# Kernel tuning notes

Measured on AMD Instinct MI355X. Metric: run time of the kernel, lower is better.

## Reference

```python
import jax, jax.numpy as jnp
import numpy as np

D_MODEL = 256
OUT_DIM = 256
D_STATE = 16
D_CONV = 4
EXPAND = 2
D_INNER = EXPAND * D_MODEL  # 512
DT_RANK = (D_MODEL + 15) // 16  # 16
B_SZ, L = 2, 4096


def setup_inputs() -> dict:
    key = jax.random.key(0)
    ks = jax.random.split(key, 12)
    s = lambda *sh: 0.02
    inp = {}
    inp['x'] = jax.random.normal(ks[0], (B_SZ, L, D_MODEL), jnp.float32)
    inp['ln_w'] = jnp.ones((D_MODEL,), jnp.float32)
    inp['ln_b'] = jnp.zeros((D_MODEL,), jnp.float32)
    inp['in_proj_w'] = jax.random.normal(ks[1], (2 * D_INNER, D_MODEL), jnp.float32) * 0.02
    inp['conv_w'] = jax.random.normal(ks[2], (D_INNER, 1, D_CONV), jnp.float32) * 0.2
    inp['conv_b'] = jnp.zeros((D_INNER,), jnp.float32)
    inp['x_proj_w'] = jax.random.normal(ks[3], (DT_RANK + 2 * D_STATE, D_INNER), jnp.float32) * 0.02
    inp['dt_proj_w'] = jax.random.normal(ks[4], (D_INNER, DT_RANK), jnp.float32) * 0.05
    inp['dt_proj_b'] = jax.random.uniform(ks[5], (D_INNER,), jnp.float32, -4.0, -2.0)  # small dt after softplus
    inp['A_log'] = jnp.log(jnp.broadcast_to(jnp.arange(1, D_STATE + 1, dtype=jnp.float32), (D_INNER, D_STATE)))
    inp['Dskip'] = jnp.ones((D_INNER,), jnp.float32)
    inp['out_proj_w'] = jax.random.normal(ks[6], (D_MODEL, D_INNER), jnp.float32) * 0.02
    inp['proj_w'] = jax.random.normal(ks[7], (OUT_DIM, D_MODEL), jnp.float32) * 0.02
    inp['proj_b'] = jnp.zeros((OUT_DIM,), jnp.float32)
    inp['skip_scale'] = jnp.ones((1,), jnp.float32)
    return inp


def _layernorm(x, w, b, eps=1e-5):
    mu = jnp.mean(x, axis=-1, keepdims=True)
    var = jnp.var(x, axis=-1, keepdims=True)
    return (x - mu) * jax.lax.rsqrt(var + eps) * w + b


def _selective_scan(u, delta, A, Bm, Cm, Dskip):
    # u, delta: (B,L,d); A: (d,n); Bm, Cm: (B,L,n)
    dA = jnp.exp(delta[..., None] * A)                       # (B,L,d,n)
    dBu = (delta * u)[..., None] * Bm[:, :, None, :]          # (B,L,d,n)
    h0 = jnp.zeros((u.shape[0], A.shape[0], A.shape[1]), u.dtype)

    def step(h, inp):
        dA_t, dBu_t, C_t = inp
        h = dA_t * h + dBu_t                                  # (B,d,n)
        y = jnp.einsum('bdn,bn->bd', h, C_t)
        return h, y

    xs = (dA.transpose(1, 0, 2, 3), dBu.transpose(1, 0, 2, 3), Cm.transpose(1, 0, 2))
    _, ys = jax.lax.scan(step, h0, xs)                        # (L,B,d)
    return ys.transpose(1, 0, 2) + u * Dskip


def _mamba(xn, in_proj_w, conv_w, conv_b, x_proj_w, dt_proj_w, dt_proj_b, A_log, Dskip, out_proj_w):
    # xn: (B,L,d_model)
    xz = jnp.einsum('bld,ed->ble', xn, in_proj_w)             # (B,L,2*d_inner)
    xi, z = jnp.split(xz, 2, axis=-1)
    # depthwise causal conv over L
    xc = jax.lax.conv_general_dilated(
        xi.transpose(0, 2, 1), conv_w, window_strides=(1,),
        padding=[(D_CONV - 1, 0)], feature_group_count=D_INNER,
        dimension_numbers=('NCH', 'OIH', 'NCH'))
    xc = (xc + conv_b[None, :, None]).transpose(0, 2, 1)       # (B,L,d_inner)
    xc = jax.nn.silu(xc)
    dbc = jnp.einsum('bld,ed->ble', xc, x_proj_w)             # (B,L,dt_rank+2n)
    dt, Bm, Cm = jnp.split(dbc, [DT_RANK, DT_RANK + D_STATE], axis=-1)
    delta = jax.nn.softplus(jnp.einsum('blr,dr->bld', dt, dt_proj_w) + dt_proj_b)
    A = -jnp.exp(A_log)                                       # (d_inner, n)
    y = _selective_scan(xc, delta, A, Bm, Cm, Dskip)
    y = y * jax.nn.silu(z)
    return jnp.einsum('ble,de->bld', y, out_proj_w)


def reference(x, ln_w, ln_b, in_proj_w, conv_w, conv_b, x_proj_w, dt_proj_w, dt_proj_b,
              A_log, Dskip, out_proj_w, proj_w, proj_b, skip_scale):
    x_norm = _layernorm(x, ln_w, ln_b)
    x_mamba = _mamba(x_norm, in_proj_w, conv_w, conv_b, x_proj_w, dt_proj_w, dt_proj_b,
                     A_log, Dskip, out_proj_w) + skip_scale * x
    x_mamba = _layernorm(x_mamba, ln_w, ln_b)
    return jnp.einsum('bld,od->blo', x_mamba, proj_w) + proj_b
```

## Files before the change

kernel.cpp:

```cpp
#include <hip/hip_runtime.h>
#include <hip/hip_bf16.h>

#define B_SZ   2
#define LSEQ   4096
#define NCH    256
#define CL     16
#define DROWS  16

typedef __attribute__((ext_vector_type(8))) short short8;
typedef __attribute__((ext_vector_type(4))) float f32x4;

__device__ __forceinline__ unsigned short f2bf(float f) {
  union { float f; unsigned u; } x; x.f = f;
  unsigned r = x.u + 0x7fffu + ((x.u >> 16) & 1u);
  return (unsigned short)(r >> 16);
}
__device__ __forceinline__ float bf2f(unsigned short u) {
  union { unsigned u; float f; } x; x.u = (unsigned)u << 16;
  return x.f;
}

__device__ __forceinline__ void gload_lds16(const unsigned short* g, unsigned short* l) {
  __builtin_amdgcn_global_load_lds(
      (const __attribute__((address_space(1))) unsigned int*)g,
      (__attribute__((address_space(3))) unsigned int*)l, 16, 0, 0);
}

__global__ __launch_bounds__(256) void prep_kernel(
    const float* __restrict__ x, const float* __restrict__ ln_w,
    const float* __restrict__ ln_b, unsigned short* __restrict__ xn_bf,
    const float* __restrict__ inW,  unsigned short* __restrict__ inW_bf,
    const float* __restrict__ outW, unsigned short* __restrict__ outW_bf,
    const float* __restrict__ projW, unsigned short* __restrict__ projW_bf,
    const float* __restrict__ xprojW, unsigned short* __restrict__ xprojW_bf,
    const float* __restrict__ A_log, float* __restrict__ Ar_tab)
{
  if (blockIdx.x < 2048) {
    int wv = threadIdx.x >> 6, lane = threadIdx.x & 63;
    size_t row = (size_t)blockIdx.x * 4 + wv;
    float4 v = reinterpret_cast<const float4*>(x)[row * 64 + lane];
    float s  = v.x + v.y + v.z + v.w;
    float sq = v.x*v.x + v.y*v.y + v.z*v.z + v.w*v.w;
    #pragma unroll
    for (int off = 32; off; off >>= 1) {
      s  += __shfl_xor(s,  off);
      sq += __shfl_xor(sq, off);
    }
    float mu  = s * (1.f/256.f);
    float var = sq * (1.f/256.f) - mu*mu;
    float rs  = rsqrtf(var + 1e-5f);
    float4 wv4 = reinterpret_cast<const float4*>(ln_w)[lane];
    float4 bv4 = reinterpret_cast<const float4*>(ln_b)[lane];
    ushort4 o;
    o.x = f2bf((v.x-mu)*rs*wv4.x + bv4.x);
    o.y = f2bf((v.y-mu)*rs*wv4.y + bv4.y);
    o.z = f2bf((v.z-mu)*rs*wv4.z + bv4.z);
    o.w = f2bf((v.w-mu)*rs*wv4.w + bv4.w);
    reinterpret_cast<ushort4*>(xn_bf)[row * 64 + lane] = o;
    return;
  }
  int j = (blockIdx.x - 2048) * 256 + threadIdx.x;
  const float* src; unsigned short* dst; int off;
  if (j < 65536)       { src = inW;    dst = inW_bf;    off = j; }
  else if (j < 98304)  { src = outW;   dst = outW_bf;   off = j - 65536; }
  else if (j < 114688) { src = projW;  dst = projW_bf;  off = j - 98304; }
  else if (j < 120832) { src = xprojW; dst = xprojW_bf; off = j - 114688; }
  else {
    int a = (j - 120832) * 4;
    float4 v = *reinterpret_cast<const float4*>(A_log + a);
    float4 o = {-__expf(v.x), -__expf(v.y), -__expf(v.z), -__expf(v.w)};
    *reinterpret_cast<float4*>(Ar_tab + a) = o;
    return;
  }
  float4 v = *reinterpret_cast<const float4*>(src + off*4);
  ushort4 o;
  o.x = f2bf(v.x); o.y = f2bf(v.y); o.z = f2bf(v.z); o.w = f2bf(v.w);
  *reinterpret_cast<ushort4*>(dst + off*4) = o;
}

__global__ __launch_bounds__(256) void ln_bf16_kernel(
    const unsigned short* __restrict__ in, const float* __restrict__ w,
    const float* __restrict__ b, unsigned short* __restrict__ out)
{
  int wv = threadIdx.x >> 6, lane = threadIdx.x & 63;
  size_t row = (size_t)blockIdx.x * 4 + wv;
  ushort4 uv = reinterpret_cast<const ushort4*>(in)[row * 64 + lane];
  float4 v = {bf2f(uv.x), bf2f(uv.y), bf2f(uv.z), bf2f(uv.w)};
  float s  = v.x + v.y + v.z + v.w;
  float sq = v.x*v.x + v.y*v.y + v.z*v.z + v.w*v.w;
  #pragma unroll
  for (int off = 32; off; off >>= 1) {
    s  += __shfl_xor(s,  off);
    sq += __shfl_xor(sq, off);
  }
  float mu  = s * (1.f/256.f);
  float var = sq * (1.f/256.f) - mu*mu;
  float rs  = rsqrtf(var + 1e-5f);
  float4 wv4 = reinterpret_cast<const float4*>(w)[lane];
  float4 bv4 = reinterpret_cast<const float4*>(b)[lane];
  ushort4 o;
  o.x = f2bf((v.x-mu)*rs*wv4.x + bv4.x);
  o.y = f2bf((v.y-mu)*rs*wv4.y + bv4.y);
  o.z = f2bf((v.z-mu)*rs*wv4.z + bv4.z);
  o.w = f2bf((v.w-mu)*rs*wv4.w + bv4.w);
  reinterpret_cast<ushort4*>(out)[row * 64 + lane] = o;
}

enum { EPI_NONE = 0, EPI_SKIPX = 1, EPI_BIAS = 2 };

template<int BM, int BN, int EPI, typename OT>
__global__ __launch_bounds__(256) void gemm_mfma(
    const unsigned short* __restrict__ A, const unsigned short* __restrict__ W,
    OT* __restrict__ C, int M, int N, int K,
    const float* __restrict__ X, const float* __restrict__ sscale,
    const float* __restrict__ bias)
{
  constexpr int BK = 32;
  constexpr int WM = BM / 2, WN = BN / 2;
  constexpr int AM = WM / 16, BF = WN / 16;
  constexpr int AI = BM / 64, BI = BN / 64;
  __shared__ __align__(16) unsigned short As[2][BM * BK];
  __shared__ __align__(16) unsigned short Ws[2][BN * BK];
  const int tid = threadIdx.x, lane = tid & 63, wid = tid >> 6;
  const int wr = wid >> 1, wc = wid & 1;
  const int bm = blockIdx.x * BM, bn = blockIdx.y * BN;
  const int srow = lane >> 2;
  const int skoff = (lane & 3) * 8;

  f32x4 acc[AM][BF] = {};

  auto stage = [&](int buf, int kt) {
    #pragma unroll
    for (int i = 0; i < AI; i++) {
      int rowg = (wid * AI + i) * 16;
      gload_lds16(A + (size_t)(bm + rowg + srow) * K + kt + skoff,
                  &As[buf][rowg * BK]);
    }
    #pragma unroll
    for (int i = 0; i < BI; i++) {
      int rowg = (wid * BI + i) * 16;
      gload_lds16(W + (size_t)(bn + rowg + srow) * K + kt + skoff,
                  &Ws[buf][rowg * BK]);
    }
  };

  stage(0, 0);
  __syncthreads();
  const int nt = K / BK;
  int cur = 0;
  for (int t = 0; t < nt; t++) {
    if (t + 1 < nt) stage(cur ^ 1, (t + 1) * BK);
    short8 af[AM], bfr[BF];
    #pragma unroll
    for (int i = 0; i < AM; i++)
      af[i] = *reinterpret_cast<const short8*>(
          &As[cur][(wr * WM + i * 16 + (lane & 15)) * BK + (lane >> 4) * 8]);
    #pragma unroll
    for (int j = 0; j < BF; j++)
      bfr[j] = *reinterpret_cast<const short8*>(
          &Ws[cur][(wc * WN + j * 16 + (lane & 15)) * BK + (lane >> 4) * 8]);
    #pragma unroll
    for (int i = 0; i < AM; i++)
      #pragma unroll
      for (int j = 0; j < BF; j++)
        acc[i][j] = __builtin_amdgcn_mfma_f32_16x16x32_bf16(af[i], bfr[j], acc[i][j], 0, 0, 0);
    __syncthreads();
    cur ^= 1;
  }

  float sv = 0.f;
  if constexpr (EPI == EPI_SKIPX) sv = sscale[0];

  #pragma unroll
  for (int i = 0; i < AM; i++) {
    #pragma unroll
    for (int j = 0; j < BF; j++) {
      int row0 = bm + wr * WM + i * 16 + ((lane >> 4) << 2);
      int col  = bn + wc * WN + j * 16 + (lane & 15);
      #pragma unroll
      for (int r = 0; r < 4; r++) {
        float v = acc[i][j][r];
        size_t off = (size_t)(row0 + r) * N + col;
        if constexpr (EPI == EPI_SKIPX) v += sv * X[off];
        if constexpr (EPI == EPI_BIAS)  v += bias[col];
        if constexpr (sizeof(OT) == 2) C[off] = (OT)f2bf(v);
        else                           C[off] = v;
      }
    }
  }
}

__global__ __launch_bounds__(256) void gemm_mfma48(
    const unsigned short* __restrict__ A, const unsigned short* __restrict__ W,
    float* __restrict__ C, int K)
{
  __shared__ __align__(16) unsigned short As[2][64 * 32];
  __shared__ __align__(16) unsigned short Ws[2][48 * 32];
  const int tid = threadIdx.x, lane = tid & 63, wid = tid >> 6;
  const int bm = blockIdx.x * 64;
  const int srow = lane >> 2, skoff = (lane & 3) * 8;

  f32x4 acc[3] = {};

  auto stage = [&](int buf, int kt) {
    int rowg = wid * 16;
    gload_lds16(A + (size_t)(bm + rowg + srow) * K + kt + skoff, &As[buf][rowg * 32]);
    if (wid < 3)
      gload_lds16(W + (size_t)(rowg + srow) * K + kt + skoff, &Ws[buf][rowg * 32]);
  };

  stage(0, 0);
  __syncthreads();
  const int nt = K / 32;
  int cur = 0;
  for (int t = 0; t < nt; t++) {
    if (t + 1 < nt) stage(cur ^ 1, (t + 1) * 32);
    short8 af = *reinterpret_cast<const short8*>(
        &As[cur][(wid * 16 + (lane & 15)) * 32 + (lane >> 4) * 8]);
    #pragma unroll
    for (int j = 0; j < 3; j++) {
      short8 bfr = *reinterpret_cast<const short8*>(
          &Ws[cur][(j * 16 + (lane & 15)) * 32 + (lane >> 4) * 8]);
      acc[j] = __builtin_amdgcn_mfma_f32_16x16x32_bf16(af, bfr, acc[j], 0, 0, 0);
    }
    __syncthreads();
    cur ^= 1;
  }
  int row0 = bm + wid * 16 + ((lane >> 4) << 2);
  #pragma unroll
  for (int j = 0; j < 3; j++) {
    int col = j * 16 + (lane & 15);
    #pragma unroll
    for (int r = 0; r < 4; r++)
      C[(size_t)(row0 + r) * 48 + col] = acc[j][r];
  }
}

__global__ __launch_bounds__(256) void conv_silu_kernel(
    const unsigned short* __restrict__ xz, const float* __restrict__ cw,
    const float* __restrict__ cb, unsigned short* __restrict__ xc_bf)
{
  int idx = blockIdx.x * 256 + threadIdx.x;
  int d4 = (idx & 127) << 2;
  int bt = idx >> 7;
  int t  = bt & (LSEQ - 1);
  int b  = bt >> 12;
  float a0 = cb[d4], a1 = cb[d4+1], a2 = cb[d4+2], a3 = cb[d4+3];
  float4 w0 = *reinterpret_cast<const float4*>(&cw[(d4+0)*4]);
  float4 w1 = *reinterpret_cast<const float4*>(&cw[(d4+1)*4]);
  float4 w2 = *reinterpret_cast<const float4*>(&cw[(d4+2)*4]);
  float4 w3 = *reinterpret_cast<const float4*>(&cw[(d4+3)*4]);
  const float* wp0 = (const float*)&w0;
  const float* wp1 = (const float*)&w1;
  const float* wp2 = (const float*)&w2;
  const float* wp3 = (const float*)&w3;
  #pragma unroll
  for (int j = 0; j < 4; j++) {
    int tt = t - 3 + j;
    if (tt >= 0) {
      ushort4 xv = *reinterpret_cast<const ushort4*>(&xz[((size_t)b*LSEQ + tt)*1024 + d4]);
      a0 += wp0[j]*bf2f(xv.x); a1 += wp1[j]*bf2f(xv.y);
      a2 += wp2[j]*bf2f(xv.z); a3 += wp3[j]*bf2f(xv.w);
    }
  }
  ushort4 ob;
  ob.x = f2bf(a0 / (1.f + __expf(-a0)));
  ob.y = f2bf(a1 / (1.f + __expf(-a1)));
  ob.z = f2bf(a2 / (1.f + __expf(-a2)));
  ob.w = f2bf(a3 / (1.f + __expf(-a3)));
  *reinterpret_cast<ushort4*>(&xc_bf[((size_t)b*LSEQ + t)*512 + d4]) = ob;
}

__global__ __launch_bounds__(256) void dtproj2_kernel(
    const float* __restrict__ dbc, const float* __restrict__ dpw,
    const float* __restrict__ dpb, unsigned short* __restrict__ delta_bf)
{
  const int tid = threadIdx.x;
  const int d0 = (tid & 127) << 2;
  float4 w[4][4];
  #pragma unroll
  for (int dd = 0; dd < 4; dd++) {
    const float4* wr = reinterpret_cast<const float4*>(&dpw[(d0+dd)*16]);
    w[dd][0] = wr[0]; w[dd][1] = wr[1]; w[dd][2] = wr[2]; w[dd][3] = wr[3];
  }
  float4 bias = *reinterpret_cast<const float4*>(&dpb[d0]);
  const float* bp = (const float*)&bias;
  size_t rbase = (size_t)blockIdx.x * DROWS + (tid >> 7);
  #pragma unroll 2
  for (int rr = 0; rr < DROWS; rr += 2) {
    size_t r = rbase + rr;
    const float4* dt = reinterpret_cast<const float4*>(dbc + r*48);
    float4 t0 = dt[0], t1 = dt[1], t2 = dt[2], t3 = dt[3];
    ushort4 ob;
    unsigned short* obp = (unsigned short*)&ob;
    #pragma unroll
    for (int dd = 0; dd < 4; dd++) {
      float acc = bp[dd];
      acc += t0.x*w[dd][0].x + t0.y*w[dd][0].y + t0.z*w[dd][0].z + t0.w*w[dd][0].w;
      acc += t1.x*w[dd][1].x + t1.y*w[dd][1].y + t1.z*w[dd][1].z + t1.w*w[dd][1].w;
      acc += t2.x*w[dd][2].x + t2.y*w[dd][2].y + t2.z*w[dd][2].z + t2.w*w[dd][2].w;
      acc += t3.x*w[dd][3].x + t3.y*w[dd][3].y + t3.z*w[dd][3].z + t3.w*w[dd][3].w;
      obp[dd] = f2bf(fmaxf(acc, 0.f) + log1pf(__expf(-fabsf(acc))));
    }
    *reinterpret_cast<ushort4*>(&delta_bf[r*512 + d0]) = ob;
  }
}

__global__ __launch_bounds__(256) void scanA_kernel(
    const unsigned short* __restrict__ delta_bf, const unsigned short* __restrict__ xc_bf,
    const float* __restrict__ dbc, const float* __restrict__ Ar_tab,
    unsigned short* __restrict__ hloc, float* __restrict__ Ssum)
{
  __shared__ float Bs[CL][16];
  const int tid = threadIdx.x;
  int g = blockIdx.x * 256 + tid;
  int nh = g & 1;
  int d  = (g >> 1) & 511;
  int c  = (g >> 10) & (NCH - 1);
  int b  = g >> 18;
  size_t tbase = (size_t)b * LSEQ + (size_t)c * CL;
  Bs[tid >> 4][tid & 15] = dbc[(tbase + (tid >> 4)) * 48 + 16 + (tid & 15)];
  const float4* Ap = reinterpret_cast<const float4*>(Ar_tab + d*16 + nh*8);
  float4 A0 = Ap[0], A1 = Ap[1];
  float Ar[8] = {A0.x, A0.y, A0.z, A0.w, A1.x, A1.y, A1.z, A1.w};
  float h[8] = {};
  float S = 0.f;
  __syncthreads();
  for (int t = 0; t < CL; t++) {
    size_t r = tbase + t;
    float dl = bf2f(delta_bf[r*512 + d]);
    float u  = bf2f(xc_bf[r*512 + d]);
    float du = dl * u;
    S += dl;
    float4 B0 = *reinterpret_cast<const float4*>(&Bs[t][nh*8]);
    float4 B1 = *reinterpret_cast<const float4*>(&Bs[t][nh*8 + 4]);
    float Bv[8] = {B0.x,B0.y,B0.z,B0.w, B1.x,B1.y,B1.z,B1.w};
    #pragma unroll
    for (int n = 0; n < 8; n++)
      h[n] = __expf(dl * Ar[n]) * h[n] + du * Bv[n];
  }
  size_t o = (((size_t)c * B_SZ + b) * 512 + d) * 16 + nh*8;
  short8 hs;
  #pragma unroll
  for (int n = 0; n < 8; n++) hs[n] = (short)f2bf(h[n]);
  *reinterpret_cast<short8*>(&hloc[o]) = hs;
  if (nh == 0) Ssum[((size_t)c * B_SZ + b) * 512 + d] = S;
}

__global__ __launch_bounds__(256) void scanmid2_kernel(
    const unsigned short* __restrict__ hloc, const float* __restrict__ Ssum,
    const float* __restrict__ Ar_tab, unsigned short* __restrict__ henter)
{
  int g = blockIdx.x * 256 + threadIdx.x;
  int n = g & 15, d = (g >> 4) & 511, b = g >> 13;
  float Ar = Ar_tab[d*16 + n];
  float h = 0.f;
  #pragma unroll 4
  for (int c = 0; c < NCH; c++) {
    size_t idx = ((size_t)c * B_SZ + b) * 512 + d;
    henter[idx*16 + n] = f2bf(h);
    h = __expf(Ssum[idx] * Ar) * h + bf2f(hloc[idx*16 + n]);
  }
}

__global__ __launch_bounds__(256) void scanB_kernel(
    const unsigned short* __restrict__ delta_bf, const unsigned short* __restrict__ xc_bf,
    const float* __restrict__ dbc, const float* __restrict__ Ar_tab,
    const unsigned short* __restrict__ henter, const float* __restrict__ Dskip,
    const unsigned short* __restrict__ xz, unsigned short* __restrict__ y_bf)
{
  __shared__ float Bs[CL][16];
  __shared__ float Cs[CL][16];
  const int tid = threadIdx.x;
  int g = blockIdx.x * 256 + tid;
  int nh = g & 1;
  int d  = (g >> 1) & 511;
  int c  = (g >> 10) & (NCH - 1);
  int b  = g >> 18;
  size_t tbase = (size_t)b * LSEQ + (size_t)c * CL;
  {
    int ts = tid >> 4, is = tid & 15;
    const float* row = dbc + (tbase + ts) * 48;
    Bs[ts][is] = row[16 + is];
    Cs[ts][is] = row[32 + is];
  }
  const float4* Ap = reinterpret_cast<const float4*>(Ar_tab + d*16 + nh*8);
  float4 A0 = Ap[0], A1 = Ap[1];
  float Ar[8] = {A0.x, A0.y, A0.z, A0.w, A1.x, A1.y, A1.z, A1.w};
  size_t o = (((size_t)c * B_SZ + b) * 512 + d) * 16 + nh*8;
  short8 hv = *reinterpret_cast<const short8*>(&henter[o]);
  float h[8];
  #pragma unroll
  for (int n = 0; n < 8; n++) h[n] = bf2f((unsigned short)hv[n]);
  float Dsk = Dskip[d];
  __syncthreads();
  for (int t = 0; t < CL; t++) {
    size_t r = tbase + t;
    float dl = bf2f(delta_bf[r*512 + d]);
    float u  = bf2f(xc_bf[r*512 + d]);
    float du = dl * u;
    float4 B0 = *reinterpret_cast<const float4*>(&Bs[t][nh*8]);
    float4 B1 = *reinterpret_cast<const float4*>(&Bs[t][nh*8 + 4]);
    float4 C0 = *reinterpret_cast<const float4*>(&Cs[t][nh*8]);
    float4 C1 = *reinterpret_cast<const float4*>(&Cs[t][nh*8 + 4]);
    float Bv[8] = {B0.x,B0.y,B0.z,B0.w, B1.x,B1.y,B1.z,B1.w};
    float Cv[8] = {C0.x,C0.y,C0.z,C0.w, C1.x,C1.y,C1.z,C1.w};
    float yp = 0.f;
    #pragma unroll
    for (int n = 0; n < 8; n++) {
      h[n] = __expf(dl * Ar[n]) * h[n] + du * Bv[n];
      yp += h[n] * Cv[n];
    }
    float y = yp + __shfl_xor(yp, 1);
    if (nh == 0) {
      y += u * Dsk;
      float z = bf2f(xz[r*1024 + 512 + d]);
      float sig = 1.f / (1.f + __expf(-z));
      y_bf[r*512 + d] = f2bf(y * z * sig);
    }
  }
}

extern "C" void kernel_launch(void* const* d_in, const int* in_sizes, int n_in,
                              void* d_out, int out_size, void* d_ws, size_t ws_size,
                              hipStream_t stream)
{
  const float* x      = (const float*)d_in[0];
  const float* ln_w   = (const float*)d_in[1];
  const float* ln_b   = (const float*)d_in[2];
  const float* inW    = (const float*)d_in[3];
  const float* convW  = (const float*)d_in[4];
  const float* convB  = (const float*)d_in[5];
  const float* xprojW = (const float*)d_in[6];
  const float* dtW    = (const float*)d_in[7];
  const float* dtB    = (const float*)d_in[8];
  const float* A_log  = (const float*)d_in[9];
  const float* Dskip  = (const float*)d_in[10];
  const float* outW   = (const float*)d_in[11];
  const float* projW  = (const float*)d_in[12];
  const float* projB  = (const float*)d_in[13];
  const float* skip   = (const float*)d_in[14];
  float* out = (float*)d_out;

  const size_t BL = (size_t)B_SZ * LSEQ;
  char* p = (char*)d_ws;
  unsigned short* xn_bf = (unsigned short*)p;  p += BL*256*2;
  unsigned short* xz_bf = (unsigned short*)p;  p += BL*1024*2;
  unsigned short* xc_bf = (unsigned short*)p;  p += BL*512*2;
  float* dbc    = (float*)p;                   p += BL*48*4;
  unsigned short* delta_bf = (unsigned short*)p; p += BL*512*2;
  unsigned short* hloc   = (unsigned short*)p; p += (size_t)NCH*B_SZ*512*16*2;
  unsigned short* henter = (unsigned short*)p; p += (size_t)NCH*B_SZ*512*16*2;
  float* Ssum   = (float*)p;                   p += (size_t)NCH*B_SZ*512*4;
  unsigned short* y_bf = (unsigned short*)p;   p += BL*512*2;
  unsigned short* inW_bf  = (unsigned short*)p; p += 1024*256*2;
  unsigned short* outW_bf = (unsigned short*)p; p += 256*512*2;
  unsigned short* projW_bf= (unsigned short*)p; p += 256*256*2;
  unsigned short* xprojW_bf=(unsigned short*)p; p += 48*512*2;
  float* Ar_tab = (float*)p;                   p += 512*16*4;
  unsigned short* xm_bf  = hloc;
  unsigned short* xn2_bf = xn_bf;

  prep_kernel<<<2048 + 480, 256, 0, stream>>>(
      x, ln_w, ln_b, xn_bf, inW, inW_bf, outW, outW_bf,
      projW, projW_bf, xprojW, xprojW_bf, A_log, Ar_tab);

  gemm_mfma<128,128,EPI_NONE><<<dim3(BL/128, 1024/128), 256, 0, stream>>>(
      xn_bf, inW_bf, xz_bf, (int)BL, 1024, 256, nullptr, nullptr, nullptr);

  conv_silu_kernel<<<(B_SZ*LSEQ*128)/256, 256, 0, stream>>>(xz_bf, convW, convB, xc_bf);

  gemm_mfma48<<<BL/64, 256, 0, stream>>>(xc_bf, xprojW_bf, dbc, 512);

  dtproj2_kernel<<<BL/DROWS, 256, 0, stream>>>(dbc, dtW, dtB, delta_bf);

  scanA_kernel<<<(B_SZ*NCH*512*2)/256, 256, 0, stream>>>(
      delta_bf, xc_bf, dbc, Ar_tab, hloc, Ssum);
  scanmid2_kernel<<<B_SZ*512*16/256, 256, 0, stream>>>(hloc, Ssum, Ar_tab, henter);
  scanB_kernel<<<(B_SZ*NCH*512*2)/256, 256, 0, stream>>>(
      delta_bf, xc_bf, dbc, Ar_tab, henter, Dskip, xz_bf, y_bf);

  gemm_mfma<64,64,EPI_SKIPX><<<dim3(BL/64, 256/64), 256, 0, stream>>>(
      y_bf, outW_bf, xm_bf, (int)BL, 256, 512, x, skip, nullptr);

  ln_bf16_kernel<<<BL/4, 256, 0, stream>>>(xm_bf, ln_w, ln_b, xn2_bf);

  gemm_mfma<64,64,EPI_BIAS><<<dim3(BL/64, 256/64), 256, 0, stream>>>(
      xn2_bf, projW_bf, out, (int)BL, 256, 256, nullptr, nullptr, projB);
}
```

Baseline: 233.3 us.

## Fuse dt projection into scanA and fuse out_proj, layernorm, proj into tail kernel

Removes the separate dtproj kernel by computing delta inside scanA from dbc staged in shared memory, writing delta once for scanB. Replaces the out_proj GEMM, layernorm kernel and final proj GEMM with one tail kernel that keeps the 64-row tile in LDS between stages. This cuts three launches and the global round trips of the intermediate activations. In exchange, grid parallelism in the tail drops to 128 blocks with 48KB of LDS each, and the second GEMM in the tail is not double-buffered.

```diff
diff --git a/kernel.cpp b/kernel.cpp
--- a/kernel.cpp
+++ b/kernel.cpp
@@ -5,7 +5,6 @@
 #define LSEQ   4096
 #define NCH    256
 #define CL     16
-#define DROWS  16
 
 typedef __attribute__((ext_vector_type(8))) short short8;
 typedef __attribute__((ext_vector_type(4))) float f32x4;
@@ -78,42 +77,10 @@
   *reinterpret_cast<ushort4*>(dst + off*4) = o;
 }
 
-__global__ __launch_bounds__(256) void ln_bf16_kernel(
-    const unsigned short* __restrict__ in, const float* __restrict__ w,
-    const float* __restrict__ b, unsigned short* __restrict__ out)
-{
-  int wv = threadIdx.x >> 6, lane = threadIdx.x & 63;
-  size_t row = (size_t)blockIdx.x * 4 + wv;
-  ushort4 uv = reinterpret_cast<const ushort4*>(in)[row * 64 + lane];
-  float4 v = {bf2f(uv.x), bf2f(uv.y), bf2f(uv.z), bf2f(uv.w)};
-  float s  = v.x + v.y + v.z + v.w;
-  float sq = v.x*v.x + v.y*v.y + v.z*v.z + v.w*v.w;
-  #pragma unroll
-  for (int off = 32; off; off >>= 1) {
-    s  += __shfl_xor(s,  off);
-    sq += __shfl_xor(sq, off);
-  }
-  float mu  = s * (1.f/256.f);
-  float var = sq * (1.f/256.f) - mu*mu;
-  float rs  = rsqrtf(var + 1e-5f);
-  float4 wv4 = reinterpret_cast<const float4*>(w)[lane];
-  float4 bv4 = reinterpret_cast<const float4*>(b)[lane];
-  ushort4 o;
-  o.x = f2bf((v.x-mu)*rs*wv4.x + bv4.x);
-  o.y = f2bf((v.y-mu)*rs*wv4.y + bv4.y);
-  o.z = f2bf((v.z-mu)*rs*wv4.z + bv4.z);
-  o.w = f2bf((v.w-mu)*rs*wv4.w + bv4.w);
-  reinterpret_cast<ushort4*>(out)[row * 64 + lane] = o;
-}
-
-enum { EPI_NONE = 0, EPI_SKIPX = 1, EPI_BIAS = 2 };
-
-template<int BM, int BN, int EPI, typename OT>
+template<int BM, int BN>
 __global__ __launch_bounds__(256) void gemm_mfma(
     const unsigned short* __restrict__ A, const unsigned short* __restrict__ W,
-    OT* __restrict__ C, int M, int N, int K,
-    const float* __restrict__ X, const float* __restrict__ sscale,
-    const float* __restrict__ bias)
+    unsigned short* __restrict__ C, int M, int N, int K)
 {
   constexpr int BK = 32;
   constexpr int WM = BM / 2, WN = BN / 2;
@@ -168,9 +135,6 @@
     cur ^= 1;
   }
 
-  float sv = 0.f;
-  if constexpr (EPI == EPI_SKIPX) sv = sscale[0];
-
   #pragma unroll
   for (int i = 0; i < AM; i++) {
     #pragma unroll
@@ -178,14 +142,8 @@
       int row0 = bm + wr * WM + i * 16 + ((lane >> 4) << 2);
       int col  = bn + wc * WN + j * 16 + (lane & 15);
       #pragma unroll
-      for (int r = 0; r < 4; r++) {
-        float v = acc[i][j][r];
-        size_t off = (size_t)(row0 + r) * N + col;
-        if constexpr (EPI == EPI_SKIPX) v += sv * X[off];
-        if constexpr (EPI == EPI_BIAS)  v += bias[col];
-        if constexpr (sizeof(OT) == 2) C[off] = (OT)f2bf(v);
-        else                           C[off] = v;
-      }
+      for (int r = 0; r < 4; r++)
+        C[(size_t)(row0 + r) * N + col] = f2bf(acc[i][j][r]);
     }
   }
 }
@@ -271,46 +229,14 @@
   *reinterpret_cast<ushort4*>(&xc_bf[((size_t)b*LSEQ + t)*512 + d4]) = ob;
 }
 
-__global__ __launch_bounds__(256) void dtproj2_kernel(
-    const float* __restrict__ dbc, const float* __restrict__ dpw,
-    const float* __restrict__ dpb, unsigned short* __restrict__ delta_bf)
-{
-  const int tid = threadIdx.x;
-  const int d0 = (tid & 127) << 2;
-  float4 w[4][4];
-  #pragma unroll
-  for (int dd = 0; dd < 4; dd++) {
-    const float4* wr = reinterpret_cast<const float4*>(&dpw[(d0+dd)*16]);
-    w[dd][0] = wr[0]; w[dd][1] = wr[1]; w[dd][2] = wr[2]; w[dd][3] = wr[3];
-  }
-  float4 bias = *reinterpret_cast<const float4*>(&dpb[d0]);
-  const float* bp = (const float*)&bias;
-  size_t rbase = (size_t)blockIdx.x * DROWS + (tid >> 7);
-  #pragma unroll 2
-  for (int rr = 0; rr < DROWS; rr += 2) {
-    size_t r = rbase + rr;
-    const float4* dt = reinterpret_cast<const float4*>(dbc + r*48);
-    float4 t0 = dt[0], t1 = dt[1], t2 = dt[2], t3 = dt[3];
-    ushort4 ob;
-    unsigned short* obp = (unsigned short*)&ob;
-    #pragma unroll
-    for (int dd = 0; dd < 4; dd++) {
-      float acc = bp[dd];
-      acc += t0.x*w[dd][0].x + t0.y*w[dd][0].y + t0.z*w[dd][0].z + t0.w*w[dd][0].w;
-      acc += t1.x*w[dd][1].x + t1.y*w[dd][1].y + t1.z*w[dd][1].z + t1.w*w[dd][1].w;
-      acc += t2.x*w[dd][2].x + t2.y*w[dd][2].y + t2.z*w[dd][2].z + t2.w*w[dd][2].w;
-      acc += t3.x*w[dd][3].x + t3.y*w[dd][3].y + t3.z*w[dd][3].z + t3.w*w[dd][3].w;
-      obp[dd] = f2bf(fmaxf(acc, 0.f) + log1pf(__expf(-fabsf(acc))));
-    }
-    *reinterpret_cast<ushort4*>(&delta_bf[r*512 + d0]) = ob;
-  }
-}
-
 __global__ __launch_bounds__(256) void scanA_kernel(
-    const unsigned short* __restrict__ delta_bf, const unsigned short* __restrict__ xc_bf,
-    const float* __restrict__ dbc, const float* __restrict__ Ar_tab,
+    const unsigned short* __restrict__ xc_bf, const float* __restrict__ dbc,
+    const float* __restrict__ Ar_tab,
+    const float* __restrict__ dtW, const float* __restrict__ dtB,
+    unsigned short* __restrict__ delta_bf,
     unsigned short* __restrict__ hloc, float* __restrict__ Ssum)
 {
+  __shared__ float dts[CL][16];
   __shared__ float Bs[CL][16];
   const int tid = threadIdx.x;
   int g = blockIdx.x * 256 + tid;
@@ -319,16 +245,42 @@
   int c  = (g >> 10) & (NCH - 1);
   int b  = g >> 18;
   size_t tbase = (size_t)b * LSEQ + (size_t)c * CL;
-  Bs[tid >> 4][tid & 15] = dbc[(tbase + (tid >> 4)) * 48 + 16 + (tid & 15)];
+  {
+    int ts = tid >> 4, is = tid & 15;
+    const float* row = dbc + (tbase + ts) * 48;
+    dts[ts][is] = row[is];
+    Bs[ts][is]  = row[16 + is];
+  }
+  const float4* wp = reinterpret_cast<const float4*>(dtW + d*16);
+  float4 w0 = wp[0], w1 = wp[1], w2 = wp[2], w3 = wp[3];
+  float dbias = dtB[d];
   const float4* Ap = reinterpret_cast<const float4*>(Ar_tab + d*16 + nh*8);
   float4 A0 = Ap[0], A1 = Ap[1];
   float Ar[8] = {A0.x, A0.y, A0.z, A0.w, A1.x, A1.y, A1.z, A1.w};
+  __syncthreads();
+  float dlv[CL];
+  #pragma unroll
+  for (int t = 0; t < CL; t++) {
+    float4 t0 = *reinterpret_cast<const float4*>(&dts[t][0]);
+    float4 t1 = *reinterpret_cast<const float4*>(&dts[t][4]);
+    float4 t2 = *reinterpret_cast<const float4*>(&dts[t][8]);
+    float4 t3 = *reinterpret_cast<const float4*>(&dts[t][12]);
+    float acc = dbias;
+    acc += t0.x*w0.x + t0.y*w0.y + t0.z*w0.z + t0.w*w0.w;
+    acc += t1.x*w1.x + t1.y*w1.y + t1.z*w1.z + t1.w*w1.w;
+    acc += t2.x*w2.x + t2.y*w2.y + t2.z*w2.z + t2.w*w2.w;
+    acc += t3.x*w3.x + t3.y*w3.y + t3.z*w3.z + t3.w*w3.w;
+    float sp = fmaxf(acc, 0.f) + log1pf(__expf(-fabsf(acc)));
+    unsigned short dl16 = f2bf(sp);
+    dlv[t] = bf2f(dl16);
+    if (nh == 0) delta_bf[(tbase + t)*512 + d] = dl16;
+  }
   float h[8] = {};
   float S = 0.f;
-  __syncthreads();
+  #pragma unroll
   for (int t = 0; t < CL; t++) {
     size_t r = tbase + t;
-    float dl = bf2f(delta_bf[r*512 + d]);
+    float dl = dlv[t];
     float u  = bf2f(xc_bf[r*512 + d]);
     float du = dl * u;
     S += dl;
@@ -417,6 +369,139 @@
       float z = bf2f(xz[r*1024 + 512 + d]);
       float sig = 1.f / (1.f + __expf(-z));
       y_bf[r*512 + d] = f2bf(y * z * sig);
+    }
+  }
+}
+
+__global__ __launch_bounds__(256) void tail_kernel(
+    const unsigned short* __restrict__ Y, const unsigned short* __restrict__ Wo,
+    const float* __restrict__ X, const float* __restrict__ sscale,
+    const float* __restrict__ ln_w, const float* __restrict__ ln_b,
+    const unsigned short* __restrict__ Wp, const float* __restrict__ projB,
+    float* __restrict__ out)
+{
+  __shared__ __align__(16) unsigned short tlds[24576];
+  const int tid = threadIdx.x, lane = tid & 63, wid = tid >> 6;
+  const int wr = wid >> 1, wc = wid & 1;
+  const int bm = blockIdx.x * 64;
+  const int srow = lane >> 2, skoff = (lane & 3) * 8;
+  const int q = lane >> 4;
+
+  f32x4 acc[2][8] = {};
+
+  auto stage1 = [&](int buf, int kt) {
+    int rowg = wid * 16;
+    gload_lds16(Y + (size_t)(bm + rowg + srow) * 512 + kt + skoff,
+                &tlds[buf * 2048 + rowg * 32]);
+    #pragma unroll
+    for (int i = 0; i < 4; i++) {
+      int rw = (wid * 4 + i) * 16;
+      gload_lds16(Wo + (size_t)(rw + srow) * 512 + kt + skoff,
+                  &tlds[4096 + buf * 8192 + rw * 32]);
+    }
+  };
+
+  stage1(0, 0);
+  __syncthreads();
+  int cur = 0;
+  for (int t = 0; t < 16; t++) {
+    if (t + 1 < 16) stage1(cur ^ 1, (t + 1) * 32);
+    short8 af[2], bfr[8];
+    #pragma unroll
+    for (int i = 0; i < 2; i++)
+      af[i] = *reinterpret_cast<const short8*>(
+          &tlds[cur * 2048 + (wr * 32 + i * 16 + (lane & 15)) * 32 + q * 8]);
+    #pragma unroll
+    for (int j = 0; j < 8; j++)
+      bfr[j] = *reinterpret_cast<const short8*>(
+          &tlds[4096 + cur * 8192 + (wc * 128 + j * 16 + (lane & 15)) * 32 + q * 8]);
+    #pragma unroll
+    for (int i = 0; i < 2; i++)
+      #pragma unroll
+      for (int j = 0; j < 8; j++)
+        acc[i][j] = __builtin_amdgcn_mfma_f32_16x16x32_bf16(af[i], bfr[j], acc[i][j], 0, 0, 0);
+    __syncthreads();
+    cur ^= 1;
+  }
+
+  float sv = sscale[0];
+  #pragma unroll
+  for (int i = 0; i < 2; i++) {
+    #pragma unroll
+    for (int j = 0; j < 8; j++) {
+      int lrow0 = wr * 32 + i * 16 + q * 4;
+      int col   = wc * 128 + j * 16 + (lane & 15);
+      #pragma unroll
+      for (int r = 0; r < 4; r++) {
+        float v = acc[i][j][r] + sv * X[(size_t)(bm + lrow0 + r) * 256 + col];
+        tlds[(lrow0 + r) * 256 + col] = f2bf(v);
+      }
+    }
+  }
+  __syncthreads();
+
+  float4 wv4 = reinterpret_cast<const float4*>(ln_w)[lane];
+  float4 bv4 = reinterpret_cast<const float4*>(ln_b)[lane];
+  for (int rr = 0; rr < 16; rr++) {
+    int row = wid * 16 + rr;
+    ushort4 uv = *reinterpret_cast<const ushort4*>(&tlds[row * 256 + lane * 4]);
+    float4 v = {bf2f(uv.x), bf2f(uv.y), bf2f(uv.z), bf2f(uv.w)};
+    float s  = v.x + v.y + v.z + v.w;
+    float sq = v.x*v.x + v.y*v.y + v.z*v.z + v.w*v.w;
+    #pragma unroll
+    for (int off = 32; off; off >>= 1) {
+      s  += __shfl_xor(s,  off);
+      sq += __shfl_xor(sq, off);
+    }
+    float mu  = s * (1.f/256.f);
+    float var = sq * (1.f/256.f) - mu*mu;
+    float rs  = rsqrtf(var + 1e-5f);
+    ushort4 o;
+    o.x = f2bf((v.x-mu)*rs*wv4.x + bv4.x);
+    o.y = f2bf((v.y-mu)*rs*wv4.y + bv4.y);
+    o.z = f2bf((v.z-mu)*rs*wv4.z + bv4.z);
+    o.w = f2bf((v.w-mu)*rs*wv4.w + bv4.w);
+    *reinterpret_cast<ushort4*>(&tlds[row * 256 + lane * 4]) = o;
+  }
+  __syncthreads();
+
+  f32x4 acc2[2][8] = {};
+  for (int t2 = 0; t2 < 8; t2++) {
+    int kt = t2 * 32;
+    #pragma unroll
+    for (int i = 0; i < 4; i++) {
+      int rw = (wid * 4 + i) * 16;
+      gload_lds16(Wp + (size_t)(rw + srow) * 256 + kt + skoff,
+                  &tlds[16384 + rw * 32]);
+    }
+    __syncthreads();
+    short8 af2[2], bfr2[8];
+    #pragma unroll
+    for (int i = 0; i < 2; i++)
+      af2[i] = *reinterpret_cast<const short8*>(
+          &tlds[(wr * 32 + i * 16 + (lane & 15)) * 256 + kt + q * 8]);
+    #pragma unroll
+    for (int j = 0; j < 8; j++)
+      bfr2[j] = *reinterpret_cast<const short8*>(
+          &tlds[16384 + (wc * 128 + j * 16 + (lane & 15)) * 32 + q * 8]);
+    #pragma unroll
+    for (int i = 0; i < 2; i++)
+      #pragma unroll
+      for (int j = 0; j < 8; j++)
+        acc2[i][j] = __builtin_amdgcn_mfma_f32_16x16x32_bf16(af2[i], bfr2[j], acc2[i][j], 0, 0, 0);
+    __syncthreads();
+  }
+
+  #pragma unroll
+  for (int i = 0; i < 2; i++) {
+    #pragma unroll
+    for (int j = 0; j < 8; j++) {
+      int row0 = bm + wr * 32 + i * 16 + q * 4;
+      int col  = wc * 128 + j * 16 + (lane & 15);
+      float bb = projB[col];
+      #pragma unroll
+      for (int r = 0; r < 4; r++)
+        out[(size_t)(row0 + r) * 256 + col] = acc2[i][j][r] + bb;
     }
   }
 }
@@ -458,33 +543,24 @@
   unsigned short* projW_bf= (unsigned short*)p; p += 256*256*2;
   unsigned short* xprojW_bf=(unsigned short*)p; p += 48*512*2;
   float* Ar_tab = (float*)p;                   p += 512*16*4;
-  unsigned short* xm_bf  = hloc;
-  unsigned short* xn2_bf = xn_bf;
 
   prep_kernel<<<2048 + 480, 256, 0, stream>>>(
       x, ln_w, ln_b, xn_bf, inW, inW_bf, outW, outW_bf,
       projW, projW_bf, xprojW, xprojW_bf, A_log, Ar_tab);
 
-  gemm_mfma<128,128,EPI_NONE><<<dim3(BL/128, 1024/128), 256, 0, stream>>>(
-      xn_bf, inW_bf, xz_bf, (int)BL, 1024, 256, nullptr, nullptr, nullptr);
+  gemm_mfma<128,128><<<dim3(BL/128, 1024/128), 256, 0, stream>>>(
+      xn_bf, inW_bf, xz_bf, (int)BL, 1024, 256);
 
   conv_silu_kernel<<<(B_SZ*LSEQ*128)/256, 256, 0, stream>>>(xz_bf, convW, convB, xc_bf);
 
   gemm_mfma48<<<BL/64, 256, 0, stream>>>(xc_bf, xprojW_bf, dbc, 512);
 
-  dtproj2_kernel<<<BL/DROWS, 256, 0, stream>>>(dbc, dtW, dtB, delta_bf);
-
   scanA_kernel<<<(B_SZ*NCH*512*2)/256, 256, 0, stream>>>(
-      delta_bf, xc_bf, dbc, Ar_tab, hloc, Ssum);
+      xc_bf, dbc, Ar_tab, dtW, dtB, delta_bf, hloc, Ssum);
   scanmid2_kernel<<<B_SZ*512*16/256, 256, 0, stream>>>(hloc, Ssum, Ar_tab, henter);
   scanB_kernel<<<(B_SZ*NCH*512*2)/256, 256, 0, stream>>>(
       delta_bf, xc_bf, dbc, Ar_tab, henter, Dskip, xz_bf, y_bf);
 
-  gemm_mfma<64,64,EPI_SKIPX><<<dim3(BL/64, 256/64), 256, 0, stream>>>(
-      y_bf, outW_bf, xm_bf, (int)BL, 256, 512, x, skip, nullptr);
-
-  ln_bf16_kernel<<<BL/4, 256, 0, stream>>>(xm_bf, ln_w, ln_b, xn2_bf);
-
-  gemm_mfma<64,64,EPI_BIAS><<<dim3(BL/64, 256/64), 256, 0, stream>>>(
-      xn2_bf, projW_bf, out, (int)BL, 256, 256, nullptr, nullptr, projB);
-}
+  tail_kernel<<<BL/64, 256, 0, stream>>>(
+      y_bf, outW_bf, x, skip, ln_w, ln_b, projW_bf, projB, out);
+}
```

New measurement: 250.2 us. +7.2%, slower.
